# Optimization experiments

Measured on AMD Instinct MI355X. Metric: run time of the kernel, lower is better.

## Reference

```python
import jax, jax.numpy as jnp
import numpy as np

BN_EPS = 1e-5


def conv1x1(x, W, b):
    # x: [B, Cin, N], W: [Cout, Cin], b: [Cout]
    return jnp.einsum('oc,bcn->bon', W, x) + b[None, :, None]


def bn(x, p):
    # p: [4, C] rows = gamma, beta, running_mean, running_var (inference BN)
    g, be, m, v = p[0], p[1], p[2], p[3]
    inv = jax.lax.rsqrt(v + BN_EPS)
    return (x - m[None, :, None]) * (g * inv)[None, :, None] + be[None, :, None]


def conv_bn_relu(x, W, b, p):
    return jax.nn.relu(bn(conv1x1(x, W, b), p))


def _make_params(key, cout, cin):
    k1, k2 = jax.random.split(key)
    W = jax.random.normal(k1, (cout, cin), jnp.float32) * (1.0 / np.sqrt(cin))
    b = jax.random.normal(k2, (cout,), jnp.float32) * 0.01
    p = jnp.stack([jnp.ones(cout), jnp.zeros(cout), jnp.zeros(cout), jnp.ones(cout)]).astype(jnp.float32)
    return W, b, p


def setup_inputs() -> dict:
    key = jax.random.key(0)
    ks = jax.random.split(key, 16)
    B, N, S, D1, D2 = 2, 16384, 4096, 128, 256
    Cin, C, Cm = D1 + D2 + 13, 128, 128  # 397, out_channel, mlp[0]
    inp = {
        'xyz1': jax.random.normal(ks[0], (B, N, 3), jnp.float32),
        'xyz2': jax.random.normal(ks[1], (B, S, 3), jnp.float32),
        'points1': jax.random.normal(ks[2], (B, D1, N), jnp.float32),
        'points2': jax.random.normal(ks[3], (B, D2, S), jnp.float32),
        'last_pred': jax.random.normal(ks[4], (B, S, 13), jnp.float32),
    }
    inp['fuse_W'], inp['fuse_b'], inp['fuse_bn'] = _make_params(ks[5], C, Cin)
    inp['ext1_W'], inp['ext1_b'], inp['ext1_bn'] = _make_params(ks[6], C, C)
    inp['ext2_W'], inp['ext2_b'], inp['ext2_bn'] = _make_params(ks[7], C, C)
    inp['pred1_W'], inp['pred1_b'], inp['pred1_bn'] = _make_params(ks[8], Cm, C)
    inp['pred2_W'], inp['pred2_b'], inp['pred2_bn'] = _make_params(ks[9], 13, Cm)
    return inp


def _forward(xyz1, xyz2, points1, points2, last_pred,
             fuse_W, fuse_b, fuse_bn, ext1_W, ext1_b, ext1_bn,
             ext2_W, ext2_b, ext2_bn, pred1_W, pred1_b, pred1_bn,
             pred2_W, pred2_b, pred2_bn):
    B, N, _ = xyz1.shape
    p1 = jnp.transpose(points1, (0, 2, 1))  # [B, N, D1]
    p2 = jnp.transpose(points2, (0, 2, 1))  # [B, S, D2]
    # squared distances [B, N, S]
    dists = (jnp.sum(xyz1 ** 2, -1)[:, :, None]
             + jnp.sum(xyz2 ** 2, -1)[:, None, :]
             - 2.0 * jnp.einsum('bnc,bsc->bns', xyz1, xyz2))
    # 3 smallest distances (partial top-k instead of full sort; same math)
    neg_d3, idx = jax.lax.top_k(-dists, 3)  # [B, N, 3]
    d3 = -neg_d3
    recip = 1.0 / (d3 + 1e-8)
    weight = recip / jnp.sum(recip, axis=2, keepdims=True)  # [B, N, 3]
    bidx = jnp.arange(B)[:, None, None]
    interp_pts = jnp.sum(p2[bidx, idx] * weight[..., None], axis=2)        # [B, N, D2]
    interp_pred = jnp.sum(last_pred[bidx, idx] * weight[..., None], axis=2)  # [B, N, 13]
    new_points = jnp.transpose(jnp.concatenate([p1, interp_pts, interp_pred], axis=-1), (0, 2, 1))  # [B, Cin, N]
    # fuse
    x = conv_bn_relu(new_points, fuse_W, fuse_b, fuse_bn)
    # extraction: one ConvBNReLURes1D block (groups=1, res_expansion=1)
    h = conv_bn_relu(x, ext1_W, ext1_b, ext1_bn)
    x = jax.nn.relu(bn(conv1x1(h, ext2_W, ext2_b), ext2_bn) + x)  # [B, C, N]
    new_points_out = x
    # prediction head (dropout is identity in eval mode)
    feat = conv_bn_relu(x, pred1_W, pred1_b, pred1_bn)
    pred = conv_bn_relu(feat, pred2_W, pred2_b, pred2_bn)
    return (new_points_out,
            jnp.transpose(feat, (0, 2, 1)),
            jnp.transpose(pred, (0, 2, 1)))


def reference(xyz1, xyz2, points1, points2, last_pred,
              fuse_W, fuse_b, fuse_bn, ext1_W, ext1_b, ext1_bn,
              ext2_W, ext2_b, ext2_bn, pred1_W, pred1_b, pred1_bn,
              pred2_W, pred2_b, pred2_bn):
    return _forward(xyz1, xyz2, points1, points2, last_pred,
                    fuse_W, fuse_b, fuse_bn, ext1_W, ext1_b, ext1_bn,
                    ext2_W, ext2_b, ext2_bn, pred1_W, pred1_b, pred1_bn,
                    pred2_W, pred2_b, pred2_bn)
```

## Files before the change

kernel.cpp:

```cpp
#include <hip/hip_runtime.h>
#include <stdint.h>

#define B_   2
#define N_   16384
#define S_   4096
#define D2_  256
#define CIN_ 397
#define KP_  416
#define C_   128
#define OC_  13
#define NCHUNK_ 16
#define CHS_ (S_ / NCHUNK_)
#define NCAND_ (NCHUNK_ * 3)
#define XBI_P 296

typedef unsigned short u16;
typedef unsigned int u32;
typedef short s16x8 __attribute__((ext_vector_type(8)));
typedef float f32x4 __attribute__((ext_vector_type(4)));

#define MFMA16(a, b, c) __builtin_amdgcn_mfma_f32_16x16x32_bf16((a), (b), (c), 0, 0, 0)

__device__ __forceinline__ float b2f(u16 h) {
  union { unsigned int u; float f; } v; v.u = ((unsigned int)h) << 16; return v.f;
}
__device__ __forceinline__ u16 f2b(float f) {
  union { float f; unsigned int u; } v; v.f = f;
  unsigned int r = v.u + 0x7fffu + ((v.u >> 16) & 1u);
  return (u16)(r >> 16);
}

#define INS3U32(k0, k1, k2, key)            \
  do {                                      \
    u32 _t1 = max(k0, key);                 \
    u32 _t2 = max(k1, key);                 \
    k0 = min(k0, key);                      \
    k1 = min(k1, _t1);                      \
    k2 = min(k2, _t2);                      \
  } while (0)

__device__ __forceinline__ void transpose_body(
    const float* __restrict__ in, u16* __restrict__ out,
    int C, int S, int opitch, int b, int s0, int c0,
    float* __restrict__ tile, int tr, int tc4) {
  const float* ip = in + (size_t)b * C * S;
  u16* op = out + (size_t)b * S * opitch;
#pragma unroll
  for (int r = 0; r < 64; r += 16) {
    float4 v = *(const float4*)(ip + (size_t)(c0 + tr + r) * S + s0 + tc4);
    tile[(tr + r) * 65 + tc4 + 0] = v.x;
    tile[(tr + r) * 65 + tc4 + 1] = v.y;
    tile[(tr + r) * 65 + tc4 + 2] = v.z;
    tile[(tr + r) * 65 + tc4 + 3] = v.w;
  }
  __syncthreads();
#pragma unroll
  for (int r = 0; r < 64; r += 16) {
    ushort4 v;
    v.x = f2b(tile[(tc4 + 0) * 65 + tr + r]);
    v.y = f2b(tile[(tc4 + 1) * 65 + tr + r]);
    v.z = f2b(tile[(tc4 + 2) * 65 + tr + r]);
    v.w = f2b(tile[(tc4 + 3) * 65 + tr + r]);
    *(ushort4*)(op + (size_t)(s0 + tr + r) * opitch + c0 + tc4) = v;
  }
}

__global__ __launch_bounds__(256) void setup_scan_kernel(
    const float* __restrict__ xyz1, const float* __restrict__ xyz2,
    const float* __restrict__ points1, const float* __restrict__ points2,
    const float* __restrict__ fW, const float* __restrict__ fb,
    const float* __restrict__ fbn,
    const float* __restrict__ e1W, const float* __restrict__ e1b,
    const float* __restrict__ e1bn,
    const float* __restrict__ e2W, const float* __restrict__ e2b,
    const float* __restrict__ e2bn,
    const float* __restrict__ p1W, const float* __restrict__ p1b,
    const float* __restrict__ p1bn,
    const float* __restrict__ p2W, const float* __restrict__ p2b,
    const float* __restrict__ p2bn,
    u16* __restrict__ cand, u16* __restrict__ npT, u16* __restrict__ p2t,
    u16* __restrict__ Wf, u16* __restrict__ W1o,
    u16* __restrict__ W2o, u16* __restrict__ W3o,
    u16* __restrict__ Wp2, float* __restrict__ st) {
  __shared__ __align__(16) float smem[64 * 65];
  int id = blockIdx.x;
  int tid = threadIdx.x;

  if (id < 1024) {
    float4* pts = (float4*)smem;
    int chunk = id & 15;
    int ny = (id >> 4) & 31;
    int b = id >> 9;
    int s0 = chunk * CHS_;
    const float* x2 = xyz2 + ((size_t)b * S_ + s0) * 3;
    {
      float xx = x2[tid * 3], yy = x2[tid * 3 + 1], zz = x2[tid * 3 + 2];
      pts[tid] = make_float4(xx, yy, zz, fmaf(xx, xx, fmaf(yy, yy, zz * zz)));
// ... 31 lines not shown
      INS3U32(d0, d1, d2, kbB);
    }
    INS3U32(a0, a1, a2, b0);
    INS3U32(a0, a1, a2, b1);
    INS3U32(a0, a1, a2, b2);
    INS3U32(c0, c1, c2, d0);
    INS3U32(c0, c1, c2, d1);
    INS3U32(c0, c1, c2, d2);
    u16* coA = cand + ((size_t)(b * N_ + nA)) * NCAND_ + chunk * 3;
    coA[0] = (u16)((a0 & 0xFFu) + s0);
    coA[1] = (u16)((a1 & 0xFFu) + s0);
    coA[2] = (u16)((a2 & 0xFFu) + s0);
    u16* coB = cand + ((size_t)(b * N_ + nB)) * NCAND_ + chunk * 3;
    coB[0] = (u16)((c0 & 0xFFu) + s0);
    coB[1] = (u16)((c1 & 0xFFu) + s0);
    coB[2] = (u16)((c2 & 0xFFu) + s0);
    return;
  }

  int tr = tid >> 4;
  int tc4 = (tid & 15) * 4;
  if (id < 2048) {
    int id2 = id - 1024;
    int sx = id2 & 255, sy = (id2 >> 8) & 1, b = id2 >> 9;
    transpose_body(points1, npT, 128, N_, 128, b, sx * 64, sy * 64, smem, tr, tc4);
    return;
  }
  if (id < 2560) {
    int id2 = id - 2048;
    int sx = id2 & 63, sy = (id2 >> 6) & 3, b = id2 >> 8;
    transpose_body(points2, p2t, 256, S_, 256, b, sx * 64, sy * 64, smem, tr, tc4);
    return;
  }
  int t = (id - 2560) * 256 + tid;
  int stride = 64 * 256;
  for (int i = t; i < 128 * KP_; i += stride) {
    int m = i / KP_, k = i - m * KP_;
    Wf[i] = (k < CIN_) ? f2b(fW[m * CIN_ + k]) : (u16)0;
  }
  for (int i = t; i < 128 * 128; i += stride) {
    W1o[i] = f2b(e1W[i]);
    W2o[i] = f2b(e2W[i]);
    W3o[i] = f2b(p1W[i]);
  }
  for (int i = t; i < 16 * 128; i += stride) {
    int m = i >> 7;
    Wp2[i] = (m < OC_) ? f2b(p2W[i]) : (u16)0;
  }
  for (int i = t; i < 5 * 128; i += stride) {
    int sg = i >> 7, c = i & 127;
    const float* bn; const float* bc; int Cc = 128;
    switch (sg) {
      case 0: bn = fbn;  bc = fb;  break;
      case 1: bn = e1bn; bc = e1b; break;
      case 2: bn = e2bn; bc = e2b; break;
      case 3: bn = p1bn; bc = p1b; break;
      default: bn = p2bn; bc = p2b; Cc = OC_; break;
    }
    float s = 0.f, tt = 0.f;
    if (c < Cc) {
      float g  = bn[0 * Cc + c], be = bn[1 * Cc + c];
      float mu = bn[2 * Cc + c], vv = bn[3 * Cc + c];
      float inv = 1.0f / sqrtf(vv + 1e-5f);
      s = g * inv;
      tt = (bc[c] - mu) * s + be;
    }
    st[sg * 256 + c] = s;
    st[sg * 256 + 128 + c] = tt;
  }
}

__device__ __forceinline__ void ins3(double d, int i,
                                     double& D0, double& D1, double& D2,
                                     int& I0, int& I1, int& I2) {
  if ((d < D2) || (d == D2 && i < I2)) {
    if ((d < D1) || (d == D1 && i < I1)) {
      D2 = D1; I2 = I1;
      if ((d < D0) || (d == D0 && i < I0)) { D1 = D0; I1 = I0; D0 = d; I0 = i; }
      else                                  { D1 = d; I1 = i; }
    } else { D2 = d; I2 = i; }
  }
}

__device__ __forceinline__ void gemm32(const u16* __restrict__ W, const u16* xb,
                                       int l15, int lq, int wv, f32x4 acc[2][2]) {
#pragma unroll
  for (int mtl = 0; mtl < 2; ++mtl) {
    acc[mtl][0] = (f32x4){0.f, 0.f, 0.f, 0.f};
    acc[mtl][1] = (f32x4){0.f, 0.f, 0.f, 0.f};
  }
#pragma unroll
  for (int ks = 0; ks < 4; ++ks) {
    int ko = ks * 32 + lq * 8;
    s16x8 b0 = *(const s16x8*)(xb + l15 * 136 + ko);
    s16x8 b1 = *(const s16x8*)(xb + (16 + l15) * 136 + ko);
#pragma unroll
    for (int mtl = 0; mtl < 2; ++mtl) {
      s16x8 a = *(const s16x8*)(W + (size_t)((wv * 2 + mtl) * 16 + l15) * 128 + ko);
      acc[mtl][0] = MFMA16(a, b0, acc[mtl][0]);
      acc[mtl][1] = MFMA16(a, b1, acc[mtl][1]);
    }
  }
}

__global__ __launch_bounds__(256, 4) void mega_kernel(
    const float* __restrict__ xyz1, const float* __restrict__ xyz2,
    const u16* __restrict__ cand,
    const u16* __restrict__ npT, const u16* __restrict__ p2t,
    const float* __restrict__ last_pred,
    const u16* __restrict__ Wf,
    const u16* __restrict__ W1, const u16* __restrict__ W2,
    const u16* __restrict__ W3, const u16* __restrict__ Wp2,
    const float* __restrict__ st, float* __restrict__ out) {
  __shared__ __align__(16) u16 xb0[32 * 136];
  __shared__ __align__(16) u16 xb1[32 * 136];
  __shared__ u16 xbi[32 * XBI_P];
  int b = blockIdx.y;
  int n0 = blockIdx.x * 32;
  int tid = threadIdx.x;
  int wv = tid >> 6, lane = tid & 63;
  int l15 = lane & 15, lq = lane >> 4;
  f32x4 acc[2][2];

  const u16* brow0 = npT + ((size_t)(b * N_ + n0 + l15)) * 128;
  const u16* brow1 = brow0 + (size_t)16 * 128;
  s16x8 pf0[4], pf1[4];
#pragma unroll
  for (int ks = 0; ks < 4; ++ks) {
    int ko = ks * 32 + lq * 8;
    pf0[ks] = *(const s16x8*)(brow0 + ko);
    pf1[ks] = *(const s16x8*)(brow1 + ko);
  }
  __builtin_amdgcn_sched_barrier(0);

  double D0, D1, D2v;
  int I0, I1, I2;
  float w0f, w1f, w2f;
  {
#pragma clang fp contract(off)
    int qi = tid >> 3, part = tid & 7;
    int qg = b * N_ + n0 + qi;
    const u16* ci = cand + (size_t)qg * NCAND_ + part * 6;
    const float* x2b = xyz2 + (size_t)b * S_ * 3;
    int ii[6];
#pragma unroll
    for (int j = 0; j < 6; ++j) ii[j] = ci[j];
    float pcx[6], pcy[6], pcz[6];
#pragma unroll
    for (int j = 0; j < 6; ++j) {
      const float* p = x2b + (size_t)ii[j] * 3;
      pcx[j] = p[0]; pcy[j] = p[1]; pcz[j] = p[2];
    }
    __builtin_amdgcn_sched_barrier(0);
    const float* x1 = xyz1 + (size_t)qg * 3;
    double ax = x1[0], ay = x1[1], az = x1[2];
    double n1 = (ax * ax + ay * ay) + az * az;
    D0 = 1e300; D1 = 1e300; D2v = 1e300;
    I0 = 2147483647; I1 = 2147483647; I2 = 2147483647;
#pragma unroll
    for (int j = 0; j < 6; ++j) {
      double px = pcx[j], py = pcy[j], pz = pcz[j];
      double n2 = (px * px + py * py) + pz * pz;
      double dot = (ax * px + ay * py) + az * pz;
      double d = (n1 + n2) - 2.0 * dot;
      ins3(d, ii[j], D0, D1, D2v, I0, I1, I2);
    }
#pragma unroll
    for (int r = 0; r < 3; ++r) {
      int m = 1 << r;
      double e0 = __shfl_xor(D0, m);
      double e1 = __shfl_xor(D1, m);
      double e2 = __shfl_xor(D2v, m);
      int j0 = __shfl_xor(I0, m);
      int j1 = __shfl_xor(I1, m);
      int j2 = __shfl_xor(I2, m);
      ins3(e0, j0, D0, D1, D2v, I0, I1, I2);
      ins3(e1, j1, D0, D1, D2v, I0, I1, I2);
      ins3(e2, j2, D0, D1, D2v, I0, I1, I2);
    }
    double r0 = 1.0 / (D0 + 1e-8);
    double r1 = 1.0 / (D1 + 1e-8);
    double r2 = 1.0 / (D2v + 1e-8);
    double sum = (r0 + r1) + r2;
    w0f = (float)(r0 / sum);
    w1f = (float)(r1 / sum);
    w2f = (float)(r2 / sum);
  }

  {
    const float* lpb = last_pred + (size_t)b * S_ * OC_;
    const u16* p2b = p2t + (size_t)b * S_ * D2_;
    ushort4 g0[8], g1[8], g2[8];
#pragma unroll
    for (int i = 0; i < 8; ++i) {
      int i0 = __builtin_amdgcn_readlane(I0, i * 8);
      int i1 = __builtin_amdgcn_readlane(I1, i * 8);
      int i2 = __builtin_amdgcn_readlane(I2, i * 8);
      g0[i] = *(const ushort4*)(p2b + (size_t)i0 * D2_ + lane * 4);
      g1[i] = *(const ushort4*)(p2b + (size_t)i1 * D2_ + lane * 4);
      g2[i] = *(const ushort4*)(p2b + (size_t)i2 * D2_ + lane * 4);
    }
    __builtin_amdgcn_sched_barrier(0);
#pragma unroll
    for (int i = 0; i < 8; ++i) {
      int p = wv * 8 + i;
      float w0 = __uint_as_float(__builtin_amdgcn_readlane(__float_as_uint(w0f), i * 8));
      float w1 = __uint_as_float(__builtin_amdgcn_readlane(__float_as_uint(w1f), i * 8));
      float w2 = __uint_as_float(__builtin_amdgcn_readlane(__float_as_uint(w2f), i * 8));
      int i0 = __builtin_amdgcn_readlane(I0, i * 8);
      int i1 = __builtin_amdgcn_readlane(I1, i * 8);
      int i2 = __builtin_amdgcn_readlane(I2, i * 8);
      ushort4 v;
      v.x = f2b((w0 * b2f(g0[i].x) + w1 * b2f(g1[i].x)) + w2 * b2f(g2[i].x));
      v.y = f2b((w0 * b2f(g0[i].y) + w1 * b2f(g1[i].y)) + w2 * b2f(g2[i].y));
      v.z = f2b((w0 * b2f(g0[i].z) + w1 * b2f(g1[i].z)) + w2 * b2f(g2[i].z));
      v.w = f2b((w0 * b2f(g0[i].w) + w1 * b2f(g1[i].w)) + w2 * b2f(g2[i].w));
      *(ushort4*)(&xbi[p * XBI_P + lane * 4]) = v;
      u16 pv = 0;
      if (lane < OC_) {
        pv = f2b((w0 * lpb[(size_t)i0 * OC_ + lane] + w1 * lpb[(size_t)i1 * OC_ + lane])
                 + w2 * lpb[(size_t)i2 * OC_ + lane]);
      }
      if (lane < 32) xbi[p * XBI_P + 256 + lane] = pv;
    }
  }
  __syncthreads();

#pragma unroll
  for (int mtl = 0; mtl < 2; ++mtl) {
    acc[mtl][0] = (f32x4){0.f, 0.f, 0.f, 0.f};
    acc[mtl][1] = (f32x4){0.f, 0.f, 0.f, 0.f};
  }
  {
#pragma unroll
    for (int ks = 0; ks < 4; ++ks) {
      int ko = ks * 32 + lq * 8;
#pragma unroll
      for (int mtl = 0; mtl < 2; ++mtl) {
        s16x8 a = *(const s16x8*)(Wf + (size_t)((wv * 2 + mtl) * 16 + l15) * KP_ + ko);
        acc[mtl][0] = MFMA16(a, pf0[ks], acc[mtl][0]);
        acc[mtl][1] = MFMA16(a, pf1[ks], acc[mtl][1]);
      }
    }
#pragma unroll 1
    for (int ks = 0; ks < 9; ++ks) {
      int kk = ks * 32 + lq * 8;
      s16x8 bf0 = *(const s16x8*)(&xbi[l15 * XBI_P + kk]);
      s16x8 bf1 = *(const s16x8*)(&xbi[(16 + l15) * XBI_P + kk]);
#pragma unroll
      for (int mtl = 0; mtl < 2; ++mtl) {
        s16x8 a = *(const s16x8*)(Wf + (size_t)((wv * 2 + mtl) * 16 + l15) * KP_ + 128 + kk);
        acc[mtl][0] = MFMA16(a, bf0, acc[mtl][0]);
        acc[mtl][1] = MFMA16(a, bf1, acc[mtl][1]);
      }
    }
  }
#pragma unroll
  for (int mtl = 0; mtl < 2; ++mtl) {
    int m4 = (wv * 2 + mtl) * 16 + lq * 4;
    f32x4 sc = *(const f32x4*)(st + 0 * 256 + m4);
    f32x4 bi = *(const f32x4*)(st + 0 * 256 + 128 + m4);
#pragma unroll
    for (int nt = 0; nt < 2; ++nt) {
      int n_l = nt * 16 + l15;
      ushort4 v;
      v.x = f2b(fmaxf(acc[mtl][nt][0] * sc[0] + bi[0], 0.f));
      v.y = f2b(fmaxf(acc[mtl][nt][1] * sc[1] + bi[1], 0.f));
      v.z = f2b(fmaxf(acc[mtl][nt][2] * sc[2] + bi[2], 0.f));
      v.w = f2b(fmaxf(acc[mtl][nt][3] * sc[3] + bi[3], 0.f));
      *(ushort4*)(&xb0[n_l * 136 + m4]) = v;
    }
  }
  __syncthreads();

  gemm32(W1, xb0, l15, lq, wv, acc);
#pragma unroll
  for (int mtl = 0; mtl < 2; ++mtl) {
    int m4 = (wv * 2 + mtl) * 16 + lq * 4;
    f32x4 sc = *(const f32x4*)(st + 1 * 256 + m4);
    f32x4 bi = *(const f32x4*)(st + 1 * 256 + 128 + m4);
#pragma unroll
    for (int nt = 0; nt < 2; ++nt) {
      int n_l = nt * 16 + l15;
      ushort4 v;
      v.x = f2b(fmaxf(acc[mtl][nt][0] * sc[0] + bi[0], 0.f));
      v.y = f2b(fmaxf(acc[mtl][nt][1] * sc[1] + bi[1], 0.f));
      v.z = f2b(fmaxf(acc[mtl][nt][2] * sc[2] + bi[2], 0.f));
      v.w = f2b(fmaxf(acc[mtl][nt][3] * sc[3] + bi[3], 0.f));
      *(ushort4*)(&xb1[n_l * 136 + m4]) = v;
    }
  }
  __syncthreads();

  gemm32(W2, xb1, l15, lq, wv, acc);
#pragma unroll
  for (int mtl = 0; mtl < 2; ++mtl) {
    int m4 = (wv * 2 + mtl) * 16 + lq * 4;
    f32x4 sc = *(const f32x4*)(st + 2 * 256 + m4);
    f32x4 bi = *(const f32x4*)(st + 2 * 256 + 128 + m4);
#pragma unroll
    for (int nt = 0; nt < 2; ++nt) {
      int n_l = nt * 16 + l15;
      int n_g = n0 + n_l;
      ushort4 xp = *(const ushort4*)(&xb0[n_l * 136 + m4]);
      float v0 = fmaxf(acc[mtl][nt][0] * sc[0] + bi[0] + b2f(xp.x), 0.f);
      float v1 = fmaxf(acc[mtl][nt][1] * sc[1] + bi[1] + b2f(xp.y), 0.f);
      float v2 = fmaxf(acc[mtl][nt][2] * sc[2] + bi[2] + b2f(xp.z), 0.f);
      float v3 = fmaxf(acc[mtl][nt][3] * sc[3] + bi[3] + b2f(xp.w), 0.f);
      ushort4 v;
      v.x = f2b(v0); v.y = f2b(v1); v.z = f2b(v2); v.w = f2b(v3);
      *(ushort4*)(&xb0[n_l * 136 + m4]) = v;
      out[((size_t)(b * C_ + m4 + 0)) * N_ + n_g] = v0;
      out[((size_t)(b * C_ + m4 + 1)) * N_ + n_g] = v1;
      out[((size_t)(b * C_ + m4 + 2)) * N_ + n_g] = v2;
      out[((size_t)(b * C_ + m4 + 3)) * N_ + n_g] = v3;
    }
  }
  __syncthreads();

  gemm32(W3, xb0, l15, lq, wv, acc);
  {
    float* out1 = out + (size_t)B_ * C_ * N_;
#pragma unroll
    for (int mtl = 0; mtl < 2; ++mtl) {
      int m4 = (wv * 2 + mtl) * 16 + lq * 4;
      f32x4 sc = *(const f32x4*)(st + 3 * 256 + m4);
      f32x4 bi = *(const f32x4*)(st + 3 * 256 + 128 + m4);
#pragma unroll
      for (int nt = 0; nt < 2; ++nt) {
        int n_l = nt * 16 + l15;
        int n_g = n0 + n_l;
        float v0 = fmaxf(acc[mtl][nt][0] * sc[0] + bi[0], 0.f);
        float v1 = fmaxf(acc[mtl][nt][1] * sc[1] + bi[1], 0.f);
        float v2 = fmaxf(acc[mtl][nt][2] * sc[2] + bi[2], 0.f);
        float v3 = fmaxf(acc[mtl][nt][3] * sc[3] + bi[3], 0.f);
        ushort4 v;
        v.x = f2b(v0); v.y = f2b(v1); v.z = f2b(v2); v.w = f2b(v3);
        *(ushort4*)(&xb1[n_l * 136 + m4]) = v;
        float4 o4 = make_float4(v0, v1, v2, v3);
        *(float4*)(out1 + ((size_t)(b * N_ + n_g)) * 128 + m4) = o4;
      }
    }
  }
  __syncthreads();

  if (wv < 2) {
    f32x4 a2 = (f32x4){0.f, 0.f, 0.f, 0.f};
#pragma unroll
    for (int ks = 0; ks < 4; ++ks) {
      int ko = ks * 32 + lq * 8;
      s16x8 b0 = *(const s16x8*)(&xb1[(wv * 16 + l15) * 136 + ko]);
      s16x8 a = *(const s16x8*)(Wp2 + (size_t)l15 * 128 + ko);
      a2 = MFMA16(a, b0, a2);
    }
    float* out2 = out + (size_t)B_ * C_ * N_ + (size_t)B_ * N_ * 128;
    f32x4 sc = *(const f32x4*)(st + 4 * 256 + lq * 4);
    f32x4 bi = *(const f32x4*)(st + 4 * 256 + 128 + lq * 4);
    int n_g = n0 + wv * 16 + l15;
#pragma unroll
    for (int r = 0; r < 4; ++r) {
      int m = lq * 4 + r;
      if (m < OC_) {
        out2[((size_t)(b * N_ + n_g)) * OC_ + m] =
            fmaxf(a2[r] * sc[r] + bi[r], 0.f);
      }
    }
  }
}

extern "C" void kernel_launch(void* const* d_in, const int* in_sizes, int n_in,
                              void* d_out, int out_size, void* d_ws, size_t ws_size,
                              hipStream_t stream) {
  const float* xyz1      = (const float*)d_in[0];
  const float* xyz2      = (const float*)d_in[1];
  const float* points1   = (const float*)d_in[2];
  const float* points2   = (const float*)d_in[3];
  const float* last_pred = (const float*)d_in[4];
  const float* fuse_W    = (const float*)d_in[5];
  const float* fuse_b    = (const float*)d_in[6];
  const float* fuse_bn   = (const float*)d_in[7];
  const float* ext1_W    = (const float*)d_in[8];
  const float* ext1_b    = (const float*)d_in[9];
  const float* ext1_bn   = (const float*)d_in[10];
  const float* ext2_W    = (const float*)d_in[11];
  const float* ext2_b    = (const float*)d_in[12];
  const float* ext2_bn   = (const float*)d_in[13];
  const float* pred1_W   = (const float*)d_in[14];
  const float* pred1_b   = (const float*)d_in[15];
  const float* pred1_bn  = (const float*)d_in[16];
  const float* pred2_W   = (const float*)d_in[17];
  const float* pred2_b   = (const float*)d_in[18];
  const float* pred2_bn  = (const float*)d_in[19];

  char* ws = (char*)d_ws;
  u16*   npT  = (u16*)(ws + 0);
  u16*   p2t  = (u16*)(ws + 8388608);
  u16*   cand = (u16*)(ws + 12582912);
  u16*   Wf   = (u16*)(ws + 15728640);
  u16*   W1   = (u16*)(ws + 15835136);
  u16*   W2   = (u16*)(ws + 15867904);
  u16*   W3   = (u16*)(ws + 15900672);
  u16*   Wp2  = (u16*)(ws + 15933440);
  float* st   = (float*)(ws + 15937536);

  setup_scan_kernel<<<dim3(2624), dim3(256), 0, stream>>>(
      xyz1, xyz2, points1, points2,
      fuse_W, fuse_b, fuse_bn, ext1_W, ext1_b, ext1_bn, ext2_W, ext2_b, ext2_bn,
      pred1_W, pred1_b, pred1_bn, pred2_W, pred2_b, pred2_bn,
      cand, npT, p2t, Wf, W1, W2, W3, Wp2, st);

  mega_kernel<<<dim3(N_ / 32, B_), dim3(256), 0, stream>>>(
      xyz1, xyz2, cand, npT, p2t, last_pred,
      Wf, W1, W2, W3, Wp2, st, (float*)d_out);
}
```

Before: 207.1 us.

## Make each wave own 16 points independently, removing block-level barriers

The fused kernel is restructured so each wave processes its own 16 query points through the whole chain (interpolation, fuse GEMM, residual block, heads). Each wave gets a private LDS arena, and all __syncthreads calls are removed. Each wave now computes all 128 output channels, with 8 MFMA tiles per wave instead of 2x2. Blocks now cover 64 points, and the candidate top-3 search uses 4 lanes per query with 12 candidates each. This trades barrier stalls and cross-wave coupling for more accumulator registers, reduced occupancy (launch bound 3), and re-reading every weight row per wave.

```diff
diff --git a/kernel.cpp b/kernel.cpp
--- a/kernel.cpp
+++ b/kernel.cpp
@@ -12,7 +12,12 @@
 #define NCHUNK_ 16
 #define CHS_ (S_ / NCHUNK_)
 #define NCAND_ (NCHUNK_ * 3)
-#define XBI_P 296
+
+#define XB_P   132
+#define XBI_P  292
+#define XB_SZ  (16 * XB_P)
+#define XBI_SZ (16 * XBI_P)
+#define ARENA  (XB_SZ + XBI_SZ)
 
 typedef unsigned short u16;
 typedef unsigned int u32;
@@ -210,28 +215,23 @@
   }
 }
 
-__device__ __forceinline__ void gemm32(const u16* __restrict__ W, const u16* xb,
-                                       int l15, int lq, int wv, f32x4 acc[2][2]) {
-#pragma unroll
-  for (int mtl = 0; mtl < 2; ++mtl) {
-    acc[mtl][0] = (f32x4){0.f, 0.f, 0.f, 0.f};
-    acc[mtl][1] = (f32x4){0.f, 0.f, 0.f, 0.f};
-  }
+__device__ __forceinline__ void gemm16(const u16* __restrict__ W, const u16* xb,
+                                       int l15, int lq, f32x4 acc[8]) {
+#pragma unroll
+  for (int mt = 0; mt < 8; ++mt) acc[mt] = (f32x4){0.f, 0.f, 0.f, 0.f};
 #pragma unroll
   for (int ks = 0; ks < 4; ++ks) {
     int ko = ks * 32 + lq * 8;
-    s16x8 b0 = *(const s16x8*)(xb + l15 * 136 + ko);
-    s16x8 b1 = *(const s16x8*)(xb + (16 + l15) * 136 + ko);
-#pragma unroll
-    for (int mtl = 0; mtl < 2; ++mtl) {
-      s16x8 a = *(const s16x8*)(W + (size_t)((wv * 2 + mtl) * 16 + l15) * 128 + ko);
-      acc[mtl][0] = MFMA16(a, b0, acc[mtl][0]);
-      acc[mtl][1] = MFMA16(a, b1, acc[mtl][1]);
-    }
-  }
-}
-
-__global__ __launch_bounds__(256, 4) void mega_kernel(
+    s16x8 b0 = *(const s16x8*)(xb + l15 * XB_P + ko);
+#pragma unroll
+    for (int mt = 0; mt < 8; ++mt) {
+      s16x8 a = *(const s16x8*)(W + (size_t)(mt * 16 + l15) * 128 + ko);
+      acc[mt] = MFMA16(a, b0, acc[mt]);
+    }
+  }
+}
+
+__global__ __launch_bounds__(256, 3) void mega_kernel(
     const float* __restrict__ xyz1, const float* __restrict__ xyz2,
     const u16* __restrict__ cand,
     const u16* __restrict__ npT, const u16* __restrict__ p2t,
@@ -240,25 +240,21 @@
     const u16* __restrict__ W1, const u16* __restrict__ W2,
     const u16* __restrict__ W3, const u16* __restrict__ Wp2,
     const float* __restrict__ st, float* __restrict__ out) {
-  __shared__ __align__(16) u16 xb0[32 * 136];
-  __shared__ __align__(16) u16 xb1[32 * 136];
-  __shared__ u16 xbi[32 * XBI_P];
+  __shared__ __align__(16) u16 lds_arena[4 * ARENA];
   int b = blockIdx.y;
-  int n0 = blockIdx.x * 32;
   int tid = threadIdx.x;
   int wv = tid >> 6, lane = tid & 63;
   int l15 = lane & 15, lq = lane >> 4;
-  f32x4 acc[2][2];
-
-  const u16* brow0 = npT + ((size_t)(b * N_ + n0 + l15)) * 128;
-  const u16* brow1 = brow0 + (size_t)16 * 128;
-  s16x8 pf0[4], pf1[4];
-#pragma unroll
-  for (int ks = 0; ks < 4; ++ks) {
-    int ko = ks * 32 + lq * 8;
-    pf0[ks] = *(const s16x8*)(brow0 + ko);
-    pf1[ks] = *(const s16x8*)(brow1 + ko);
-  }
+  int n0 = blockIdx.x * 64 + wv * 16;
+  u16* xb0 = lds_arena + wv * ARENA;
+  u16* xbi = xb0 + XB_SZ;
+  u16* xb1 = xbi;
+  f32x4 acc[8];
+
+  const u16* brow = npT + ((size_t)(b * N_ + n0 + l15)) * 128;
+  s16x8 pf[4];
+#pragma unroll
+  for (int ks = 0; ks < 4; ++ks) pf[ks] = *(const s16x8*)(brow + ks * 32 + lq * 8);
   __builtin_amdgcn_sched_barrier(0);
 
   double D0, D1, D2v;
@@ -266,16 +262,18 @@
   float w0f, w1f, w2f;
   {
 #pragma clang fp contract(off)
-    int qi = tid >> 3, part = tid & 7;
+    int qi = lane >> 2, part = lane & 3;
     int qg = b * N_ + n0 + qi;
-    const u16* ci = cand + (size_t)qg * NCAND_ + part * 6;
+    const u16* ci = cand + (size_t)qg * NCAND_ + part * 12;
+    ushort4 ca = *(const ushort4*)(ci);
+    ushort4 cb = *(const ushort4*)(ci + 4);
+    ushort4 cc = *(const ushort4*)(ci + 8);
+    int ii[12] = {ca.x, ca.y, ca.z, ca.w, cb.x, cb.y, cb.z, cb.w,
+                  cc.x, cc.y, cc.z, cc.w};
     const float* x2b = xyz2 + (size_t)b * S_ * 3;
-    int ii[6];
-#pragma unroll
-    for (int j = 0; j < 6; ++j) ii[j] = ci[j];
-    float pcx[6], pcy[6], pcz[6];
-#pragma unroll
-    for (int j = 0; j < 6; ++j) {
+    float pcx[12], pcy[12], pcz[12];
+#pragma unroll
+    for (int j = 0; j < 12; ++j) {
       const float* p = x2b + (size_t)ii[j] * 3;
       pcx[j] = p[0]; pcy[j] = p[1]; pcz[j] = p[2];
     }
@@ -286,7 +284,7 @@
     D0 = 1e300; D1 = 1e300; D2v = 1e300;
     I0 = 2147483647; I1 = 2147483647; I2 = 2147483647;
 #pragma unroll
-    for (int j = 0; j < 6; ++j) {
+    for (int j = 0; j < 12; ++j) {
       double px = pcx[j], py = pcy[j], pz = pcz[j];
       double n2 = (px * px + py * py) + pz * pz;
       double dot = (ax * px + ay * py) + az * pz;
@@ -294,7 +292,7 @@
       ins3(d, ii[j], D0, D1, D2v, I0, I1, I2);
     }
 #pragma unroll
-    for (int r = 0; r < 3; ++r) {
+    for (int r = 0; r < 2; ++r) {
       int m = 1 << r;
       double e0 = __shfl_xor(D0, m);
       double e1 = __shfl_xor(D1, m);
@@ -318,173 +316,148 @@
   {
     const float* lpb = last_pred + (size_t)b * S_ * OC_;
     const u16* p2b = p2t + (size_t)b * S_ * D2_;
-    ushort4 g0[8], g1[8], g2[8];
-#pragma unroll
-    for (int i = 0; i < 8; ++i) {
-      int i0 = __builtin_amdgcn_readlane(I0, i * 8);
-      int i1 = __builtin_amdgcn_readlane(I1, i * 8);
-      int i2 = __builtin_amdgcn_readlane(I2, i * 8);
-      g0[i] = *(const ushort4*)(p2b + (size_t)i0 * D2_ + lane * 4);
-      g1[i] = *(const ushort4*)(p2b + (size_t)i1 * D2_ + lane * 4);
-      g2[i] = *(const ushort4*)(p2b + (size_t)i2 * D2_ + lane * 4);
-    }
-    __builtin_amdgcn_sched_barrier(0);
-#pragma unroll
-    for (int i = 0; i < 8; ++i) {
-      int p = wv * 8 + i;
-      float w0 = __uint_as_float(__builtin_amdgcn_readlane(__float_as_uint(w0f), i * 8));
-      float w1 = __uint_as_float(__builtin_amdgcn_readlane(__float_as_uint(w1f), i * 8));
-      float w2 = __uint_as_float(__builtin_amdgcn_readlane(__float_as_uint(w2f), i * 8));
-      int i0 = __builtin_amdgcn_readlane(I0, i * 8);
-      int i1 = __builtin_amdgcn_readlane(I1, i * 8);
-      int i2 = __builtin_amdgcn_readlane(I2, i * 8);
+#pragma unroll 1
+    for (int c = 0; c < 2; ++c) {
+      int qb = c * 8;
+      ushort4 g0[8], g1[8], g2[8];
+      float lp0[8], lp1[8], lp2[8];
+#pragma unroll
+      for (int i = 0; i < 8; ++i) {
+        int i0 = __builtin_amdgcn_readlane(I0, (qb + i) * 4);
+        int i1 = __builtin_amdgcn_readlane(I1, (qb + i) * 4);
+        int i2 = __builtin_amdgcn_readlane(I2, (qb + i) * 4);
+        g0[i] = *(const ushort4*)(p2b + (size_t)i0 * D2_ + lane * 4);
+        g1[i] = *(const ushort4*)(p2b + (size_t)i1 * D2_ + lane * 4);
+        g2[i] = *(const ushort4*)(p2b + (size_t)i2 * D2_ + lane * 4);
+        if (lane < OC_) {
+          lp0[i] = lpb[(size_t)i0 * OC_ + lane];
+          lp1[i] = lpb[(size_t)i1 * OC_ + lane];
+          lp2[i] = lpb[(size_t)i2 * OC_ + lane];
+        }
+      }
+      __builtin_amdgcn_sched_barrier(0);
+#pragma unroll
+      for (int i = 0; i < 8; ++i) {
+        int p = qb + i;
+        float w0 = __uint_as_float(__builtin_amdgcn_readlane(__float_as_uint(w0f), p * 4));
+        float w1 = __uint_as_float(__builtin_amdgcn_readlane(__float_as_uint(w1f), p * 4));
+        float w2 = __uint_as_float(__builtin_amdgcn_readlane(__float_as_uint(w2f), p * 4));
+        ushort4 v;
+        v.x = f2b((w0 * b2f(g0[i].x) + w1 * b2f(g1[i].x)) + w2 * b2f(g2[i].x));
+        v.y = f2b((w0 * b2f(g0[i].y) + w1 * b2f(g1[i].y)) + w2 * b2f(g2[i].y));
+        v.z = f2b((w0 * b2f(g0[i].z) + w1 * b2f(g1[i].z)) + w2 * b2f(g2[i].z));
+        v.w = f2b((w0 * b2f(g0[i].w) + w1 * b2f(g1[i].w)) + w2 * b2f(g2[i].w));
+        *(ushort4*)(&xbi[p * XBI_P + lane * 4]) = v;
+        u16 pv = 0;
+        if (lane < OC_) pv = f2b((w0 * lp0[i] + w1 * lp1[i]) + w2 * lp2[i]);
+        if (lane < 32) xbi[p * XBI_P + 256 + lane] = pv;
+      }
+    }
+  }
+
+#pragma unroll
+  for (int mt = 0; mt < 8; ++mt) acc[mt] = (f32x4){0.f, 0.f, 0.f, 0.f};
+#pragma unroll
+  for (int ks = 0; ks < 4; ++ks) {
+    int ko = ks * 32 + lq * 8;
+#pragma unroll
+    for (int mt = 0; mt < 8; ++mt) {
+      s16x8 a = *(const s16x8*)(Wf + (size_t)(mt * 16 + l15) * KP_ + ko);
+      acc[mt] = MFMA16(a, pf[ks], acc[mt]);
+    }
+  }
+#pragma unroll 3
+  for (int ks = 0; ks < 9; ++ks) {
+    int kk = ks * 32 + lq * 8;
+    s16x8 bf = *(const s16x8*)(&xbi[l15 * XBI_P + kk]);
+#pragma unroll
+    for (int mt = 0; mt < 8; ++mt) {
+      s16x8 a = *(const s16x8*)(Wf + (size_t)(mt * 16 + l15) * KP_ + 128 + kk);
+      acc[mt] = MFMA16(a, bf, acc[mt]);
+    }
+  }
+#pragma unroll
+  for (int mt = 0; mt < 8; ++mt) {
+    int m4 = mt * 16 + lq * 4;
+    f32x4 sc = *(const f32x4*)(st + 0 * 256 + m4);
+    f32x4 bi = *(const f32x4*)(st + 0 * 256 + 128 + m4);
+    ushort4 v;
+    v.x = f2b(fmaxf(acc[mt][0] * sc[0] + bi[0], 0.f));
+    v.y = f2b(fmaxf(acc[mt][1] * sc[1] + bi[1], 0.f));
+    v.z = f2b(fmaxf(acc[mt][2] * sc[2] + bi[2], 0.f));
+    v.w = f2b(fmaxf(acc[mt][3] * sc[3] + bi[3], 0.f));
+    *(ushort4*)(&xb0[l15 * XB_P + m4]) = v;
+  }
+
+  gemm16(W1, xb0, l15, lq, acc);
+#pragma unroll
+  for (int mt = 0; mt < 8; ++mt) {
+    int m4 = mt * 16 + lq * 4;
+    f32x4 sc = *(const f32x4*)(st + 1 * 256 + m4);
+    f32x4 bi = *(const f32x4*)(st + 1 * 256 + 128 + m4);
+    ushort4 v;
+    v.x = f2b(fmaxf(acc[mt][0] * sc[0] + bi[0], 0.f));
+    v.y = f2b(fmaxf(acc[mt][1] * sc[1] + bi[1], 0.f));
+    v.z = f2b(fmaxf(acc[mt][2] * sc[2] + bi[2], 0.f));
+    v.w = f2b(fmaxf(acc[mt][3] * sc[3] + bi[3], 0.f));
+    *(ushort4*)(&xb1[l15 * XB_P + m4]) = v;
+  }
+
+  gemm16(W2, xb1, l15, lq, acc);
+#pragma unroll
+  for (int mt = 0; mt < 8; ++mt) {
+    int m4 = mt * 16 + lq * 4;
+    f32x4 sc = *(const f32x4*)(st + 2 * 256 + m4);
+    f32x4 bi = *(const f32x4*)(st + 2 * 256 + 128 + m4);
+    int n_g = n0 + l15;
+    ushort4 xp = *(const ushort4*)(&xb0[l15 * XB_P + m4]);
+    float v0 = fmaxf(acc[mt][0] * sc[0] + bi[0] + b2f(xp.x), 0.f);
+    float v1 = fmaxf(acc[mt][1] * sc[1] + bi[1] + b2f(xp.y), 0.f);
+    float v2 = fmaxf(acc[mt][2] * sc[2] + bi[2] + b2f(xp.z), 0.f);
+    float v3 = fmaxf(acc[mt][3] * sc[3] + bi[3] + b2f(xp.w), 0.f);
+    ushort4 v;
+    v.x = f2b(v0); v.y = f2b(v1); v.z = f2b(v2); v.w = f2b(v3);
+    *(ushort4*)(&xb0[l15 * XB_P + m4]) = v;
+    out[((size_t)(b * C_ + m4 + 0)) * N_ + n_g] = v0;
+    out[((size_t)(b * C_ + m4 + 1)) * N_ + n_g] = v1;
+    out[((size_t)(b * C_ + m4 + 2)) * N_ + n_g] = v2;
+    out[((size_t)(b * C_ + m4 + 3)) * N_ + n_g] = v3;
+  }
+
+  gemm16(W3, xb0, l15, lq, acc);
+  {
+    float* out1 = out + (size_t)B_ * C_ * N_;
+#pragma unroll
+    for (int mt = 0; mt < 8; ++mt) {
+      int m4 = mt * 16 + lq * 4;
+      f32x4 sc = *(const f32x4*)(st + 3 * 256 + m4);
+      f32x4 bi = *(const f32x4*)(st + 3 * 256 + 128 + m4);
+      int n_g = n0 + l15;
+      float v0 = fmaxf(acc[mt][0] * sc[0] + bi[0], 0.f);
+      float v1 = fmaxf(acc[mt][1] * sc[1] + bi[1], 0.f);
+      float v2 = fmaxf(acc[mt][2] * sc[2] + bi[2], 0.f);
+      float v3 = fmaxf(acc[mt][3] * sc[3] + bi[3], 0.f);
       ushort4 v;
-      v.x = f2b((w0 * b2f(g0[i].x) + w1 * b2f(g1[i].x)) + w2 * b2f(g2[i].x));
-      v.y = f2b((w0 * b2f(g0[i].y) + w1 * b2f(g1[i].y)) + w2 * b2f(g2[i].y));
-      v.z = f2b((w0 * b2f(g0[i].z) + w1 * b2f(g1[i].z)) + w2 * b2f(g2[i].z));
-      v.w = f2b((w0 * b2f(g0[i].w) + w1 * b2f(g1[i].w)) + w2 * b2f(g2[i].w));
-      *(ushort4*)(&xbi[p * XBI_P + lane * 4]) = v;
-      u16 pv = 0;
-      if (lane < OC_) {
-        pv = f2b((w0 * lpb[(size_t)i0 * OC_ + lane] + w1 * lpb[(size_t)i1 * OC_ + lane])
-                 + w2 * lpb[(size_t)i2 * OC_ + lane]);
-      }
-      if (lane < 32) xbi[p * XBI_P + 256 + lane] = pv;
-    }
-  }
-  __syncthreads();
-
-#pragma unroll
-  for (int mtl = 0; mtl < 2; ++mtl) {
-    acc[mtl][0] = (f32x4){0.f, 0.f, 0.f, 0.f};
-    acc[mtl][1] = (f32x4){0.f, 0.f, 0.f, 0.f};
-  }
+      v.x = f2b(v0); v.y = f2b(v1); v.z = f2b(v2); v.w = f2b(v3);
+      *(ushort4*)(&xb1[l15 * XB_P + m4]) = v;
+      float4 o4 = make_float4(v0, v1, v2, v3);
+      *(float4*)(out1 + ((size_t)(b * N_ + n_g)) * 128 + m4) = o4;
+    }
+  }
+
   {
+    f32x4 a2 = (f32x4){0.f, 0.f, 0.f, 0.f};
 #pragma unroll
     for (int ks = 0; ks < 4; ++ks) {
       int ko = ks * 32 + lq * 8;
-#pragma unroll
-      for (int mtl = 0; mtl < 2; ++mtl) {
-        s16x8 a = *(const s16x8*)(Wf + (size_t)((wv * 2 + mtl) * 16 + l15) * KP_ + ko);
-        acc[mtl][0] = MFMA16(a, pf0[ks], acc[mtl][0]);
-        acc[mtl][1] = MFMA16(a, pf1[ks], acc[mtl][1]);
-      }
-    }
-#pragma unroll 1
-    for (int ks = 0; ks < 9; ++ks) {
-      int kk = ks * 32 + lq * 8;
-      s16x8 bf0 = *(const s16x8*)(&xbi[l15 * XBI_P + kk]);
-      s16x8 bf1 = *(const s16x8*)(&xbi[(16 + l15) * XBI_P + kk]);
-#pragma unroll
-      for (int mtl = 0; mtl < 2; ++mtl) {
-        s16x8 a = *(const s16x8*)(Wf + (size_t)((wv * 2 + mtl) * 16 + l15) * KP_ + 128 + kk);
-        acc[mtl][0] = MFMA16(a, bf0, acc[mtl][0]);
-        acc[mtl][1] = MFMA16(a, bf1, acc[mtl][1]);
-      }
-    }
-  }
-#pragma unroll
-  for (int mtl = 0; mtl < 2; ++mtl) {
-    int m4 = (wv * 2 + mtl) * 16 + lq * 4;
-    f32x4 sc = *(const f32x4*)(st + 0 * 256 + m4);
-    f32x4 bi = *(const f32x4*)(st + 0 * 256 + 128 + m4);
-#pragma unroll
-    for (int nt = 0; nt < 2; ++nt) {
-      int n_l = nt * 16 + l15;
-      ushort4 v;
-      v.x = f2b(fmaxf(acc[mtl][nt][0] * sc[0] + bi[0], 0.f));
-      v.y = f2b(fmaxf(acc[mtl][nt][1] * sc[1] + bi[1], 0.f));
-      v.z = f2b(fmaxf(acc[mtl][nt][2] * sc[2] + bi[2], 0.f));
-      v.w = f2b(fmaxf(acc[mtl][nt][3] * sc[3] + bi[3], 0.f));
-      *(ushort4*)(&xb0[n_l * 136 + m4]) = v;
-    }
-  }
-  __syncthreads();
-
-  gemm32(W1, xb0, l15, lq, wv, acc);
-#pragma unroll
-  for (int mtl = 0; mtl < 2; ++mtl) {
-    int m4 = (wv * 2 + mtl) * 16 + lq * 4;
-    f32x4 sc = *(const f32x4*)(st + 1 * 256 + m4);
-    f32x4 bi = *(const f32x4*)(st + 1 * 256 + 128 + m4);
-#pragma unroll
-    for (int nt = 0; nt < 2; ++nt) {
-      int n_l = nt * 16 + l15;
-      ushort4 v;
-      v.x = f2b(fmaxf(acc[mtl][nt][0] * sc[0] + bi[0], 0.f));
-      v.y = f2b(fmaxf(acc[mtl][nt][1] * sc[1] + bi[1], 0.f));
-      v.z = f2b(fmaxf(acc[mtl][nt][2] * sc[2] + bi[2], 0.f));
-      v.w = f2b(fmaxf(acc[mtl][nt][3] * sc[3] + bi[3], 0.f));
-      *(ushort4*)(&xb1[n_l * 136 + m4]) = v;
-    }
-  }
-  __syncthreads();
-
-  gemm32(W2, xb1, l15, lq, wv, acc);
-#pragma unroll
-  for (int mtl = 0; mtl < 2; ++mtl) {
-    int m4 = (wv * 2 + mtl) * 16 + lq * 4;
-    f32x4 sc = *(const f32x4*)(st + 2 * 256 + m4);
-    f32x4 bi = *(const f32x4*)(st + 2 * 256 + 128 + m4);
-#pragma unroll
-    for (int nt = 0; nt < 2; ++nt) {
-      int n_l = nt * 16 + l15;
-      int n_g = n0 + n_l;
-      ushort4 xp = *(const ushort4*)(&xb0[n_l * 136 + m4]);
-      float v0 = fmaxf(acc[mtl][nt][0] * sc[0] + bi[0] + b2f(xp.x), 0.f);
-      float v1 = fmaxf(acc[mtl][nt][1] * sc[1] + bi[1] + b2f(xp.y), 0.f);
-      float v2 = fmaxf(acc[mtl][nt][2] * sc[2] + bi[2] + b2f(xp.z), 0.f);
-      float v3 = fmaxf(acc[mtl][nt][3] * sc[3] + bi[3] + b2f(xp.w), 0.f);
-      ushort4 v;
-      v.x = f2b(v0); v.y = f2b(v1); v.z = f2b(v2); v.w = f2b(v3);
-      *(ushort4*)(&xb0[n_l * 136 + m4]) = v;
-      out[((size_t)(b * C_ + m4 + 0)) * N_ + n_g] = v0;
-      out[((size_t)(b * C_ + m4 + 1)) * N_ + n_g] = v1;
-      out[((size_t)(b * C_ + m4 + 2)) * N_ + n_g] = v2;
-      out[((size_t)(b * C_ + m4 + 3)) * N_ + n_g] = v3;
-    }
-  }
-  __syncthreads();
-
-  gemm32(W3, xb0, l15, lq, wv, acc);
-  {
-    float* out1 = out + (size_t)B_ * C_ * N_;
-#pragma unroll
-    for (int mtl = 0; mtl < 2; ++mtl) {
-      int m4 = (wv * 2 + mtl) * 16 + lq * 4;
-      f32x4 sc = *(const f32x4*)(st + 3 * 256 + m4);
-      f32x4 bi = *(const f32x4*)(st + 3 * 256 + 128 + m4);
-#pragma unroll
-      for (int nt = 0; nt < 2; ++nt) {
-        int n_l = nt * 16 + l15;
-        int n_g = n0 + n_l;
-        float v0 = fmaxf(acc[mtl][nt][0] * sc[0] + bi[0], 0.f);
-        float v1 = fmaxf(acc[mtl][nt][1] * sc[1] + bi[1], 0.f);
-        float v2 = fmaxf(acc[mtl][nt][2] * sc[2] + bi[2], 0.f);
-        float v3 = fmaxf(acc[mtl][nt][3] * sc[3] + bi[3], 0.f);
-        ushort4 v;
-        v.x = f2b(v0); v.y = f2b(v1); v.z = f2b(v2); v.w = f2b(v3);
-        *(ushort4*)(&xb1[n_l * 136 + m4]) = v;
-        float4 o4 = make_float4(v0, v1, v2, v3);
-        *(float4*)(out1 + ((size_t)(b * N_ + n_g)) * 128 + m4) = o4;
-      }
-    }
-  }
-  __syncthreads();
-
-  if (wv < 2) {
-    f32x4 a2 = (f32x4){0.f, 0.f, 0.f, 0.f};
-#pragma unroll
-    for (int ks = 0; ks < 4; ++ks) {
-      int ko = ks * 32 + lq * 8;
-      s16x8 b0 = *(const s16x8*)(&xb1[(wv * 16 + l15) * 136 + ko]);
+      s16x8 b0 = *(const s16x8*)(&xb1[l15 * XB_P + ko]);
       s16x8 a = *(const s16x8*)(Wp2 + (size_t)l15 * 128 + ko);
       a2 = MFMA16(a, b0, a2);
     }
     float* out2 = out + (size_t)B_ * C_ * N_ + (size_t)B_ * N_ * 128;
     f32x4 sc = *(const f32x4*)(st + 4 * 256 + lq * 4);
     f32x4 bi = *(const f32x4*)(st + 4 * 256 + 128 + lq * 4);
-    int n_g = n0 + wv * 16 + l15;
+    int n_g = n0 + l15;
 #pragma unroll
     for (int r = 0; r < 4; ++r) {
       int m = lq * 4 + r;
@@ -537,7 +510,7 @@
       pred1_W, pred1_b, pred1_bn, pred2_W, pred2_b, pred2_bn,
       cand, npT, p2t, Wf, W1, W2, W3, Wp2, st);
 
-  mega_kernel<<<dim3(N_ / 32, B_), dim3(256), 0, stream>>>(
+  mega_kernel<<<dim3(N_ / 64, B_), dim3(256), 0, stream>>>(
       xyz1, xyz2, cand, npT, p2t, last_pred,
       Wf, W1, W2, W3, Wp2, st, (float*)d_out);
 }
```

New measurement: 216.1 us. 1.04x slower.

## Split fused mega kernel into separate interpolation and GEMM-chain kernels

Applied to the files above, without the earlier changes.

Splits the single fused kernel into an interpolation kernel and a GEMM kernel. The interpolation kernel does the top-3 selection, computes weights and writes the interpolated features as a bf16 row buffer to global memory. The GEMM kernel then streams those rows directly as MFMA operands instead of staging them in LDS. This drops the large shared-memory buffer and its gather latency from the GEMM kernel, which may raise occupancy. The cost is an extra kernel launch and a global write plus read of about 17 MB of intermediate data.

```diff
diff --git a/kernel.cpp b/kernel.cpp
--- a/kernel.cpp
+++ b/kernel.cpp
@@ -12,7 +12,7 @@
 #define NCHUNK_ 16
 #define CHS_ (S_ / NCHUNK_)
 #define NCAND_ (NCHUNK_ * 3)
-#define XBI_P 296
+#define XQ_P 272
 
 typedef unsigned short u16;
 typedef unsigned int u32;
@@ -210,60 +210,17 @@
   }
 }
 
-__device__ __forceinline__ void gemm32(const u16* __restrict__ W, const u16* xb,
-                                       int l15, int lq, int wv, f32x4 acc[2][2]) {
-#pragma unroll
-  for (int mtl = 0; mtl < 2; ++mtl) {
-    acc[mtl][0] = (f32x4){0.f, 0.f, 0.f, 0.f};
-    acc[mtl][1] = (f32x4){0.f, 0.f, 0.f, 0.f};
-  }
-#pragma unroll
-  for (int ks = 0; ks < 4; ++ks) {
-    int ko = ks * 32 + lq * 8;
-    s16x8 b0 = *(const s16x8*)(xb + l15 * 136 + ko);
-    s16x8 b1 = *(const s16x8*)(xb + (16 + l15) * 136 + ko);
-#pragma unroll
-    for (int mtl = 0; mtl < 2; ++mtl) {
-      s16x8 a = *(const s16x8*)(W + (size_t)((wv * 2 + mtl) * 16 + l15) * 128 + ko);
-      acc[mtl][0] = MFMA16(a, b0, acc[mtl][0]);
-      acc[mtl][1] = MFMA16(a, b1, acc[mtl][1]);
-    }
-  }
-}
-
-__global__ __launch_bounds__(256, 4) void mega_kernel(
+__global__ __launch_bounds__(256) void interp_kernel(
     const float* __restrict__ xyz1, const float* __restrict__ xyz2,
-    const u16* __restrict__ cand,
-    const u16* __restrict__ npT, const u16* __restrict__ p2t,
-    const float* __restrict__ last_pred,
-    const u16* __restrict__ Wf,
-    const u16* __restrict__ W1, const u16* __restrict__ W2,
-    const u16* __restrict__ W3, const u16* __restrict__ Wp2,
-    const float* __restrict__ st, float* __restrict__ out) {
-  __shared__ __align__(16) u16 xb0[32 * 136];
-  __shared__ __align__(16) u16 xb1[32 * 136];
-  __shared__ u16 xbi[32 * XBI_P];
-  int b = blockIdx.y;
-  int n0 = blockIdx.x * 32;
+    const u16* __restrict__ cand, const u16* __restrict__ p2t,
+    const float* __restrict__ last_pred, u16* __restrict__ xq) {
+  __shared__ int   iS[32][3];
+  __shared__ float wS[32][3];
+  int id = blockIdx.x;
+  int b = id >> 9;
+  int n0 = (id & 511) * 32;
   int tid = threadIdx.x;
-  int wv = tid >> 6, lane = tid & 63;
-  int l15 = lane & 15, lq = lane >> 4;
-  f32x4 acc[2][2];
-
-  const u16* brow0 = npT + ((size_t)(b * N_ + n0 + l15)) * 128;
-  const u16* brow1 = brow0 + (size_t)16 * 128;
-  s16x8 pf0[4], pf1[4];
-#pragma unroll
-  for (int ks = 0; ks < 4; ++ks) {
-    int ko = ks * 32 + lq * 8;
-    pf0[ks] = *(const s16x8*)(brow0 + ko);
-    pf1[ks] = *(const s16x8*)(brow1 + ko);
-  }
-  __builtin_amdgcn_sched_barrier(0);
-
-  double D0, D1, D2v;
-  int I0, I1, I2;
-  float w0f, w1f, w2f;
+
   {
 #pragma clang fp contract(off)
     int qi = tid >> 3, part = tid & 7;
@@ -279,12 +236,11 @@
       const float* p = x2b + (size_t)ii[j] * 3;
       pcx[j] = p[0]; pcy[j] = p[1]; pcz[j] = p[2];
     }
-    __builtin_amdgcn_sched_barrier(0);
     const float* x1 = xyz1 + (size_t)qg * 3;
     double ax = x1[0], ay = x1[1], az = x1[2];
     double n1 = (ax * ax + ay * ay) + az * az;
-    D0 = 1e300; D1 = 1e300; D2v = 1e300;
-    I0 = 2147483647; I1 = 2147483647; I2 = 2147483647;
+    double D0 = 1e300, D1 = 1e300, D2v = 1e300;
+    int I0 = 2147483647, I1 = 2147483647, I2 = 2147483647;
 #pragma unroll
     for (int j = 0; j < 6; ++j) {
       double px = pcx[j], py = pcy[j], pz = pcz[j];
@@ -306,78 +262,132 @@
       ins3(e1, j1, D0, D1, D2v, I0, I1, I2);
       ins3(e2, j2, D0, D1, D2v, I0, I1, I2);
     }
-    double r0 = 1.0 / (D0 + 1e-8);
-    double r1 = 1.0 / (D1 + 1e-8);
-    double r2 = 1.0 / (D2v + 1e-8);
-    double sum = (r0 + r1) + r2;
-    w0f = (float)(r0 / sum);
-    w1f = (float)(r1 / sum);
-    w2f = (float)(r2 / sum);
-  }
-
-  {
+    if (part == 0) {
+      double r0 = 1.0 / (D0 + 1e-8);
+      double r1 = 1.0 / (D1 + 1e-8);
+      double r2 = 1.0 / (D2v + 1e-8);
+      double sum = (r0 + r1) + r2;
+      wS[qi][0] = (float)(r0 / sum);
+      wS[qi][1] = (float)(r1 / sum);
+      wS[qi][2] = (float)(r2 / sum);
+      iS[qi][0] = I0; iS[qi][1] = I1; iS[qi][2] = I2;
+    }
+  }
+  __syncthreads();
+
+  int wv = tid >> 6, lane = tid & 63;
+  int q = wv * 8 + (lane >> 3);
+  int cg = lane & 7;
+  int n = n0 + q;
+  int i0 = iS[q][0], i1 = iS[q][1], i2 = iS[q][2];
+  float w0 = wS[q][0], w1 = wS[q][1], w2 = wS[q][2];
+  const u16* p2b = p2t + (size_t)b * S_ * D2_;
+  const u16* r0p = p2b + (size_t)i0 * D2_ + cg * 32;
+  const u16* r1p = p2b + (size_t)i1 * D2_ + cg * 32;
+  const u16* r2p = p2b + (size_t)i2 * D2_ + cg * 32;
+  u16* xrow = xq + (size_t)(b * N_ + n) * XQ_P;
+#pragma unroll
+  for (int j = 0; j < 8; ++j) {
+    ushort4 a = *(const ushort4*)(r0p + j * 4);
+    ushort4 e = *(const ushort4*)(r1p + j * 4);
+    ushort4 c = *(const ushort4*)(r2p + j * 4);
+    ushort4 v;
+    v.x = f2b((w0 * b2f(a.x) + w1 * b2f(e.x)) + w2 * b2f(c.x));
+    v.y = f2b((w0 * b2f(a.y) + w1 * b2f(e.y)) + w2 * b2f(c.y));
+    v.z = f2b((w0 * b2f(a.z) + w1 * b2f(e.z)) + w2 * b2f(c.z));
+    v.w = f2b((w0 * b2f(a.w) + w1 * b2f(e.w)) + w2 * b2f(c.w));
+    *(ushort4*)(xrow + cg * 32 + j * 4) = v;
+  }
+  if (cg == 0) {
     const float* lpb = last_pred + (size_t)b * S_ * OC_;
-    const u16* p2b = p2t + (size_t)b * S_ * D2_;
-    ushort4 g0[8], g1[8], g2[8];
-#pragma unroll
-    for (int i = 0; i < 8; ++i) {
-      int i0 = __builtin_amdgcn_readlane(I0, i * 8);
-      int i1 = __builtin_amdgcn_readlane(I1, i * 8);
-      int i2 = __builtin_amdgcn_readlane(I2, i * 8);
-      g0[i] = *(const ushort4*)(p2b + (size_t)i0 * D2_ + lane * 4);
-      g1[i] = *(const ushort4*)(p2b + (size_t)i1 * D2_ + lane * 4);
-      g2[i] = *(const ushort4*)(p2b + (size_t)i2 * D2_ + lane * 4);
-    }
-    __builtin_amdgcn_sched_barrier(0);
-#pragma unroll
-    for (int i = 0; i < 8; ++i) {
-      int p = wv * 8 + i;
-      float w0 = __uint_as_float(__builtin_amdgcn_readlane(__float_as_uint(w0f), i * 8));
-      float w1 = __uint_as_float(__builtin_amdgcn_readlane(__float_as_uint(w1f), i * 8));
-      float w2 = __uint_as_float(__builtin_amdgcn_readlane(__float_as_uint(w2f), i * 8));
-      int i0 = __builtin_amdgcn_readlane(I0, i * 8);
-      int i1 = __builtin_amdgcn_readlane(I1, i * 8);
-      int i2 = __builtin_amdgcn_readlane(I2, i * 8);
-      ushort4 v;
-      v.x = f2b((w0 * b2f(g0[i].x) + w1 * b2f(g1[i].x)) + w2 * b2f(g2[i].x));
-      v.y = f2b((w0 * b2f(g0[i].y) + w1 * b2f(g1[i].y)) + w2 * b2f(g2[i].y));
-      v.z = f2b((w0 * b2f(g0[i].z) + w1 * b2f(g1[i].z)) + w2 * b2f(g2[i].z));
-      v.w = f2b((w0 * b2f(g0[i].w) + w1 * b2f(g1[i].w)) + w2 * b2f(g2[i].w));
-      *(ushort4*)(&xbi[p * XBI_P + lane * 4]) = v;
-      u16 pv = 0;
-      if (lane < OC_) {
-        pv = f2b((w0 * lpb[(size_t)i0 * OC_ + lane] + w1 * lpb[(size_t)i1 * OC_ + lane])
-                 + w2 * lpb[(size_t)i2 * OC_ + lane]);
-      }
-      if (lane < 32) xbi[p * XBI_P + 256 + lane] = pv;
-    }
-  }
-  __syncthreads();
-
+    u16 pv[16];
+#pragma unroll
+    for (int c = 0; c < 16; ++c) pv[c] = 0;
+#pragma unroll
+    for (int c = 0; c < OC_; ++c) {
+      float l0 = lpb[(size_t)i0 * OC_ + c];
+      float l1 = lpb[(size_t)i1 * OC_ + c];
+      float l2 = lpb[(size_t)i2 * OC_ + c];
+      pv[c] = f2b((w0 * l0 + w1 * l1) + w2 * l2);
+    }
+#pragma unroll
+    for (int c4 = 0; c4 < 4; ++c4) {
+      *(ushort4*)(xrow + 256 + c4 * 4) =
+          make_ushort4(pv[c4 * 4], pv[c4 * 4 + 1], pv[c4 * 4 + 2], pv[c4 * 4 + 3]);
+    }
+  }
+}
+
+__device__ __forceinline__ void gemm32(const u16* __restrict__ W, const u16* xb,
+                                       int l15, int lq, int wv, f32x4 acc[2][2]) {
 #pragma unroll
   for (int mtl = 0; mtl < 2; ++mtl) {
     acc[mtl][0] = (f32x4){0.f, 0.f, 0.f, 0.f};
     acc[mtl][1] = (f32x4){0.f, 0.f, 0.f, 0.f};
   }
+#pragma unroll
+  for (int ks = 0; ks < 4; ++ks) {
+    int ko = ks * 32 + lq * 8;
+    s16x8 b0 = *(const s16x8*)(xb + l15 * 136 + ko);
+    s16x8 b1 = *(const s16x8*)(xb + (16 + l15) * 136 + ko);
+#pragma unroll
+    for (int mtl = 0; mtl < 2; ++mtl) {
+      s16x8 a = *(const s16x8*)(W + (size_t)((wv * 2 + mtl) * 16 + l15) * 128 + ko);
+      acc[mtl][0] = MFMA16(a, b0, acc[mtl][0]);
+      acc[mtl][1] = MFMA16(a, b1, acc[mtl][1]);
+    }
+  }
+}
+
+__global__ __launch_bounds__(256, 4) void gemm_kernel(
+    const u16* __restrict__ npT, const u16* __restrict__ xq,
+    const u16* __restrict__ Wf,
+    const u16* __restrict__ W1, const u16* __restrict__ W2,
+    const u16* __restrict__ W3, const u16* __restrict__ Wp2,
+    const float* __restrict__ st, float* __restrict__ out) {
+  __shared__ __align__(16) u16 xb0[32 * 136];
+  __shared__ __align__(16) u16 xb1[32 * 136];
+  int b = blockIdx.y;
+  int n0 = blockIdx.x * 32;
+  int tid = threadIdx.x;
+  int wv = tid >> 6, lane = tid & 63;
+  int l15 = lane & 15, lq = lane >> 4;
+  f32x4 acc[2][2];
+
+#pragma unroll
+  for (int mtl = 0; mtl < 2; ++mtl) {
+    acc[mtl][0] = (f32x4){0.f, 0.f, 0.f, 0.f};
+    acc[mtl][1] = (f32x4){0.f, 0.f, 0.f, 0.f};
+  }
   {
-#pragma unroll
+    const u16* brow0 = npT + ((size_t)(b * N_ + n0 + l15)) * 128;
+    const u16* brow1 = brow0 + (size_t)16 * 128;
+#pragma unroll 2
     for (int ks = 0; ks < 4; ++ks) {
       int ko = ks * 32 + lq * 8;
+      s16x8 bf0 = *(const s16x8*)(brow0 + ko);
+      s16x8 bf1 = *(const s16x8*)(brow1 + ko);
 #pragma unroll
       for (int mtl = 0; mtl < 2; ++mtl) {
         s16x8 a = *(const s16x8*)(Wf + (size_t)((wv * 2 + mtl) * 16 + l15) * KP_ + ko);
-        acc[mtl][0] = MFMA16(a, pf0[ks], acc[mtl][0]);
-        acc[mtl][1] = MFMA16(a, pf1[ks], acc[mtl][1]);
+        acc[mtl][0] = MFMA16(a, bf0, acc[mtl][0]);
+        acc[mtl][1] = MFMA16(a, bf1, acc[mtl][1]);
       }
     }
-#pragma unroll 1
+    const u16* qrow0 = xq + ((size_t)(b * N_ + n0 + l15)) * XQ_P;
+    const u16* qrow1 = qrow0 + (size_t)16 * XQ_P;
+#pragma unroll 3
     for (int ks = 0; ks < 9; ++ks) {
-      int kk = ks * 32 + lq * 8;
-      s16x8 bf0 = *(const s16x8*)(&xbi[l15 * XBI_P + kk]);
-      s16x8 bf1 = *(const s16x8*)(&xbi[(16 + l15) * XBI_P + kk]);
+      int col = ks * 32 + lq * 8;
+      s16x8 bf0 = {0, 0, 0, 0, 0, 0, 0, 0};
+      s16x8 bf1 = {0, 0, 0, 0, 0, 0, 0, 0};
+      if (ks < 8 || lq < 2) {
+        bf0 = *(const s16x8*)(qrow0 + col);
+        bf1 = *(const s16x8*)(qrow1 + col);
+      }
 #pragma unroll
       for (int mtl = 0; mtl < 2; ++mtl) {
-        s16x8 a = *(const s16x8*)(Wf + (size_t)((wv * 2 + mtl) * 16 + l15) * KP_ + 128 + kk);
+        s16x8 a = *(const s16x8*)(Wf + (size_t)((wv * 2 + mtl) * 16 + l15) * KP_ + 128 + col);
         acc[mtl][0] = MFMA16(a, bf0, acc[mtl][0]);
         acc[mtl][1] = MFMA16(a, bf1, acc[mtl][1]);
       }
@@ -530,6 +540,7 @@
   u16*   W3   = (u16*)(ws + 15900672);
   u16*   Wp2  = (u16*)(ws + 15933440);
   float* st   = (float*)(ws + 15937536);
+  u16*   xq   = (u16*)(ws + 15942656);
 
   setup_scan_kernel<<<dim3(2624), dim3(256), 0, stream>>>(
       xyz1, xyz2, points1, points2,
@@ -537,7 +548,9 @@
       pred1_W, pred1_b, pred1_bn, pred2_W, pred2_b, pred2_bn,
       cand, npT, p2t, Wf, W1, W2, W3, Wp2, st);
 
-  mega_kernel<<<dim3(N_ / 32, B_), dim3(256), 0, stream>>>(
-      xyz1, xyz2, cand, npT, p2t, last_pred,
-      Wf, W1, W2, W3, Wp2, st, (float*)d_out);
-}
+  interp_kernel<<<dim3(1024), dim3(256), 0, stream>>>(
+      xyz1, xyz2, cand, p2t, last_pred, xq);
+
+  gemm_kernel<<<dim3(N_ / 32, B_), dim3(256), 0, stream>>>(
+      npT, xq, Wf, W1, W2, W3, Wp2, st, (float*)d_out);
+}
```

New measurement: 222.1 us. +7.2%, slower.
